# Optimization experiments

Measured on AMD Instinct MI355X. Metric: run time of the kernel, lower is better.

Reference implementation:

```python
import jax, jax.numpy as jnp
import numpy as np

INPUT_SIZE = 64
ENC_HID = 128
HIDDEN = 512
NUM_CLASSES = 8
B = 512
T = 256


def setup_inputs() -> dict:
    key = jax.random.key(0)
    ks = jax.random.split(key, 12)

    def lin(k, out_f, in_f):
        bound = 1.0 / np.sqrt(in_f)
        return jax.random.uniform(k, (out_f, in_f), jnp.float32, -bound, bound)

    def bias(k, out_f, in_f):
        bound = 1.0 / np.sqrt(in_f)
        return jax.random.uniform(k, (out_f,), jnp.float32, -bound, bound)

    return {
        "sequence": jax.random.normal(ks[0], (B, T, INPUT_SIZE), jnp.float32),
        "W1": lin(ks[1], ENC_HID, INPUT_SIZE),
        "b1": bias(ks[2], ENC_HID, INPUT_SIZE),
        "W2": lin(ks[3], HIDDEN, ENC_HID),
        "b2": bias(ks[4], HIDDEN, ENC_HID),
        "W_ih": lin(ks[5], 4 * HIDDEN, HIDDEN),
        "W_hh": lin(ks[6], 4 * HIDDEN, HIDDEN),
        "b_ih": bias(ks[7], 4 * HIDDEN, HIDDEN),
        "b_hh": bias(ks[8], 4 * HIDDEN, HIDDEN),
        "Wfc": lin(ks[9], NUM_CLASSES, HIDDEN),
        "bfc": bias(ks[10], NUM_CLASSES, HIDDEN),
    }


def reference(sequence, W1, b1, W2, b2, W_ih, W_hh, b_ih, b_hh, Wfc, bfc):
    # Encoder applied to every timestep (same math as per-step in the torch loop)
    x = jnp.einsum('bti,hi->bth', sequence, W1) + b1          # [B,T,128]
    x = jnp.where(x > 0, x, 0.01 * x)                         # LeakyReLU(0.01)
    x = jnp.einsum('bth,dh->btd', x, W2) + b2                 # [B,T,H]

    Bsz = sequence.shape[0]
    H = W_hh.shape[1]

    def step(carry, xt):
        h, c = carry
        gates = xt @ W_ih.T + b_ih + h @ W_hh.T + b_hh        # [B,4H]
        i, f, g, o = jnp.split(gates, 4, axis=-1)
        i = jax.nn.sigmoid(i)
        f = jax.nn.sigmoid(f)
        g = jnp.tanh(g)
        o = jax.nn.sigmoid(o)
        c = f * c + i * g
        h = o * jnp.tanh(c)
        return (h, c), None

    h0 = jnp.zeros((Bsz, H), x.dtype)
    (h, _), _ = jax.lax.scan(step, (h0, h0), jnp.swapaxes(x, 0, 1))  # scan over T
    return h @ Wfc.T + bfc                                    # [B,num_classes]
```

## Files before the change

kernel.cpp:

```cpp
#include <hip/hip_runtime.h>
#include <cstdint>
#include <cstddef>

#define ZB 512
#define ZT 256
#define ZIN 64
#define ZEH 128
#define ZH 512
#define ZG 2048
#define ZNC 8
#define NBLK 256

typedef __attribute__((ext_vector_type(8))) short s8v;
typedef __attribute__((ext_vector_type(4))) float f4v;
typedef unsigned short u16;
typedef unsigned int u32;
typedef unsigned long long u64;

__device__ __forceinline__ u16 f2bf(float f){
  u32 u = __builtin_bit_cast(u32, f);
  u += 0x7FFFu + ((u >> 16) & 1u);
  return (u16)(u >> 16);
}
__device__ __forceinline__ s8v pair2v(u64 a, u64 b){
  union { u64 q[2]; s8v v; } u; u.q[0] = a; u.q[1] = b; return u.v;
}
__device__ __forceinline__ size_t qoff2(int buf, int bg, int hf, int hg){
  return ((((size_t)buf * 8 + bg) * 2 + hf) * 32 + hg) * 512;
}
__device__ __forceinline__ u64 aload(const u64* p){
  return __hip_atomic_load(p, __ATOMIC_RELAXED, __HIP_MEMORY_SCOPE_AGENT);
}

__global__ __launch_bounds__(128)
void k_fold(const float* __restrict__ W_ih, const float* __restrict__ W2,
            const float* __restrict__ b2, const float* __restrict__ b_ih,
            const float* __restrict__ b_hh, u16* __restrict__ Wc,
            float* __restrict__ bc)
{
  const int r = blockIdx.x, c = threadIdx.x;
  const float* wr = W_ih + (size_t)r * ZH;
  float acc = 0.f;
  for (int k = 0; k < ZH; ++k) acc += wr[k] * W2[(size_t)k * ZEH + c];
  Wc[(size_t)r * ZEH + c] = f2bf(acc);
  __shared__ float red[128];
  float p = 0.f;
  for (int k = c; k < ZH; k += 128) p += wr[k] * b2[k];
  red[c] = p; __syncthreads();
  for (int s = 64; s > 0; s >>= 1){ if (c < s) red[c] += red[c + s]; __syncthreads(); }
  if (c == 0) bc[r] = red[0] + b_ih[r] + b_hh[r];
}

__global__ __launch_bounds__(256)
void k_cvt(const float* __restrict__ src, u16* __restrict__ dst, int n)
{
  int i = blockIdx.x * 256 + threadIdx.x;
  if (i < n) dst[i] = f2bf(src[i]);
}

__global__ __launch_bounds__(256)
void k_enc(const float* __restrict__ seq, const float* __restrict__ W1,
           const float* __restrict__ b1, u16* __restrict__ X1)
{
  __shared__ float w1s[ZEH * 65];
  __shared__ float sqs[64 * 65];
  const int tid = threadIdx.x;
  const size_t rb = (size_t)blockIdx.x * 64;
  for (int i = tid; i < ZEH * ZIN; i += 256){ int r = i >> 6, c = i & 63; w1s[r * 65 + c] = W1[i]; }
  for (int i = tid; i < 64 * ZIN; i += 256){ int r = i >> 6, c = i & 63; sqs[r * 65 + c] = seq[(rb + r) * ZIN + c]; }
  __syncthreads();
  const int cg = tid & 31, rg = tid >> 5;
  float acc[8][4];
  #pragma unroll
  for (int i = 0; i < 8; ++i){
    #pragma unroll
    for (int j = 0; j < 4; ++j) acc[i][j] = 0.f;
  }
  for (int k = 0; k < ZIN; ++k){
    float wv[4], sv[8];
    #pragma unroll
    for (int j = 0; j < 4; ++j) wv[j] = w1s[(cg * 4 + j) * 65 + k];
    #pragma unroll
    for (int i = 0; i < 8; ++i) sv[i] = sqs[(rg * 8 + i) * 65 + k];
    #pragma unroll
    for (int i = 0; i < 8; ++i){
      #pragma unroll
      for (int j = 0; j < 4; ++j) acc[i][j] += sv[i] * wv[j];
    }
  }
  #pragma unroll
  for (int i = 0; i < 8; ++i){
    ushort4 pk;
    float v0 = acc[i][0] + b1[cg * 4 + 0]; v0 = v0 > 0.f ? v0 : 0.01f * v0;
    float v1 = acc[i][1] + b1[cg * 4 + 1]; v1 = v1 > 0.f ? v1 : 0.01f * v1;
    float v2 = acc[i][2] + b1[cg * 4 + 2]; v2 = v2 > 0.f ? v2 : 0.01f * v2;
    float v3 = acc[i][3] + b1[cg * 4 + 3]; v3 = v3 > 0.f ? v3 : 0.01f * v3;
    pk.x = f2bf(v0); pk.y = f2bf(v1); pk.z = f2bf(v2); pk.w = f2bf(v3);
    int rf = (int)rb + rg * 8 + i;
    int b = rf >> 8, tt = rf & 255;
    *(ushort4*)(X1 + ((size_t)tt * ZB + b) * ZEH + cg * 4) = pk;
  }
}

__device__ __forceinline__ void qwait(const u32* flags, int gidx, u32 target)
{
  const int l = threadIdx.x & 63;
  const u32* fp = flags + ((size_t)(gidx * 32 + (l & 31))) * 16;
  long long guard = 0;
  for (;;){
    u32 v = __hip_atomic_load(fp, __ATOMIC_RELAXED, __HIP_MEMORY_SCOPE_AGENT);
    if (__ballot(v >= target) == ~0ull) break;
    __builtin_amdgcn_s_sleep(1);
    if (++guard > (1LL << 20)) break;
  }
}

__global__ __launch_bounds__(512, 1)
void k_lstm(const u16* __restrict__ X1, const u16* __restrict__ Whh,
            const u16* __restrict__ Wcf, const float* __restrict__ bc,
            const u16* __restrict__ Wfcb, const float* __restrict__ bfc,
            u16* __restrict__ hbuf, float* __restrict__ out,
            u32* __restrict__ flags)
{
  __shared__ u16 hs2[2][32 * ZH];
  const int tid = threadIdx.x;
  const int bg = (int)blockIdx.x >> 5, hg = (int)blockIdx.x & 31;
  const bool isC = (tid < 256);
  const int w = (tid >> 6) & 3, l = tid & 63;
  const int lr = l & 15, lg = l >> 4;
  const int st = tid & 255;
  const int gt = lr >> 2;

  s8v bwh[16], bwx[4];
  f4v biasv = {0.f, 0.f, 0.f, 0.f};
  float c_reg[2][2][4];
  if (isC){
    const int grow = gt * ZH + hg * 16 + w * 4 + (lr & 3);
    const u16* p = Whh + (size_t)grow * ZH + lg * 8;
    #pragma unroll
    for (int kt = 0; kt < 16; ++kt) bwh[kt] = *(const s8v*)(p + kt * 32);
    const u16* q = Wcf + (size_t)grow * ZEH + lg * 8;
    #pragma unroll
    for (int kt = 0; kt < 4; ++kt) bwx[kt] = *(const s8v*)(q + kt * 32);
    float b = bc[grow];
    biasv[0] = b; biasv[1] = b; biasv[2] = b; biasv[3] = b;
    #pragma unroll
    for (int a = 0; a < 2; ++a){
      #pragma unroll
      for (int m = 0; m < 2; ++m){
        #pragma unroll
        for (int r = 0; r < 4; ++r) c_reg[a][m][r] = 0.f;
      }
    }
  }

  if (!isC){
    const u64* src = (const u64*)(hbuf + qoff2(0, bg, 0, 0));
    u64 va[8], vb[8];
    #pragma unroll
    for (int i = 0; i < 8; ++i){
      int cc = st + i * 256;
      va[i] = aload(src + (size_t)cc * 2);
      vb[i] = aload(src + (size_t)cc * 2 + 1);
    }
    #pragma unroll
    for (int i = 0; i < 8; ++i){
      int byte = (st + i * 256) * 16;
      int swz = byte ^ (((byte >> 5) & 3) << 4);
      *(s8v*)((char*)hs2[0] + swz) = pair2v(va[i], vb[i]);
    }
  }
  __syncthreads();

  u32* flbase = flags + ((size_t)(bg * 64 + hg)) * 16;

  for (int t = 0; t < ZT; ++t){
    #pragma unroll
    for (int hf = 0; hf < 2; ++hf){
      if (isC){
        s8v ax[2][4];
        #pragma unroll
        for (int m = 0; m < 2; ++m){
          const u16* xp = X1 + ((size_t)t * ZB + (bg * 64 + hf * 32 + m * 16 + lr)) * ZEH + lg * 8;
          #pragma unroll
          for (int kt = 0; kt < 4; ++kt) ax[m][kt] = *(const s8v*)(xp + kt * 32);
        }

        const char* hb = (const char*)hs2[hf];
        f4v accm[2];
        #pragma unroll
        for (int m = 0; m < 2; ++m){
          f4v a0 = biasv;
          f4v a1 = {0.f, 0.f, 0.f, 0.f};
          #pragma unroll
          for (int kt = 0; kt < 8; ++kt){
            int byte = (2 * kt + (lg >> 1)) * 1024 + (m * 16 + lr) * 32 + (lg & 1) * 16;
            byte ^= (((byte >> 5) & 3) << 4);
            s8v av = *(const s8v*)(hb + byte);
            a0 = __builtin_amdgcn_mfma_f32_16x16x32_bf16(av, bwh[kt], a0, 0, 0, 0);
          }
          #pragma unroll
          for (int kt = 8; kt < 16; ++kt){
            int byte = (2 * kt + (lg >> 1)) * 1024 + (m * 16 + lr) * 32 + (lg & 1) * 16;
            byte ^= (((byte >> 5) & 3) << 4);
            s8v av = *(const s8v*)(hb + byte);
            a1 = __builtin_amdgcn_mfma_f32_16x16x32_bf16(av, bwh[kt], a1, 0, 0, 0);
          }
          a0 = __builtin_amdgcn_mfma_f32_16x16x32_bf16(ax[m][0], bwx[0], a0, 0, 0, 0);
          a1 = __builtin_amdgcn_mfma_f32_16x16x32_bf16(ax[m][1], bwx[1], a1, 0, 0, 0);
          a0 = __builtin_amdgcn_mfma_f32_16x16x32_bf16(ax[m][2], bwx[2], a0, 0, 0, 0);
          a1 = __builtin_amdgcn_mfma_f32_16x16x32_bf16(ax[m][3], bwx[3], a1, 0, 0, 0);
          accm[m] = a0 + a1;
        }

        u16* hdst = hbuf + qoff2((t + 1) & 1, bg, hf, hg);
        #pragma unroll
        for (int m = 0; m < 2; ++m){
          #pragma unroll
          for (int r = 0; r < 4; ++r){
            float v = accm[m][r];
            float s = (gt == 2) ? 2.f : -1.f;
            float e = __expf(v * s);
            float rc = 1.f / (1.f + e);
            float a = (gt == 2) ? (1.f - 2.f * rc) : rc;
            float f_ = __shfl_xor(a, 4);
            float g_ = __shfl_xor(a, 8);
            float o_ = __shfl_xor(a, 12);
            float cv = f_ * c_reg[hf][m][r] + a * g_;
            c_reg[hf][m][r] = cv;
            float e2 = __expf(2.f * cv);
            float hv = o_ * (1.f - 2.f / (1.f + e2));
            u32 bits = f2bf(hv);
            u32 lo = bits | (((u32)__shfl_xor((int)bits, 1)) << 16);
            u32 hi = (u32)__shfl_xor((int)lo, 2);
            if (lr == 0){
              u64 pk = (u64)lo | ((u64)hi << 32);
              __hip_atomic_store((u64*)(hdst + (size_t)(m * 16 + lg * 4 + r) * 16 + w * 4), pk,
                                 __ATOMIC_RELAXED, __HIP_MEMORY_SCOPE_AGENT);
            }
          }
        }
      } else {
        const int hfT = hf ^ 1;
        const int tf  = t + hf;
        if (tf < ZT || hf == 0){
          if (!(t == 0 && hf == 0))
            qwait(flags, bg * 2 + hfT, (u32)tf);
          const u64* src = (const u64*)(hbuf + qoff2(tf & 1, bg, hfT, 0));
          u64 va[8], vb[8];
          #pragma unroll
          for (int i = 0; i < 8; ++i){
            int cc = st + i * 256;
            va[i] = aload(src + (size_t)cc * 2);
            vb[i] = aload(src + (size_t)cc * 2 + 1);
          }
          char* dst = (char*)hs2[hf ^ 1];
          #pragma unroll
          for (int i = 0; i < 8; ++i){
            int byte = (st + i * 256) * 16;
            int swz = byte ^ (((byte >> 5) & 3) << 4);
            *(s8v*)(dst + swz) = pair2v(va[i], vb[i]);
          }
        }
      }
      __syncthreads();
      if (tid == 0)
        __hip_atomic_store(flbase + (size_t)hf * 512, (u32)(t + 1),
                           __ATOMIC_RELAXED, __HIP_MEMORY_SCOPE_AGENT);
    }
  }

  if (hg == 0){
    if (tid < 64){
      qwait(flags, bg * 2 + 0, (u32)ZT);
      qwait(flags, bg * 2 + 1, (u32)ZT);
    }
    __syncthreads();
    if (isC){
      float ob = (lr < ZNC) ? bfc[lr] : 0.f;
      f4v acc = {ob, ob, ob, ob};
      const u16* wp = Wfcb + (size_t)lr * ZH + lg * 8;
      const int hfE = w >> 1;
      const int ric = (w & 1) * 16 + lr;
      #pragma unroll
      for (int kt = 0; kt < 16; ++kt){
        int hgp = 2 * kt + (lg >> 1);
        const u64* hp = (const u64*)(hbuf + qoff2(0, bg, hfE, hgp) + (size_t)ric * 16 + (lg & 1) * 8);
        u64 a0 = aload(hp);
        u64 a1 = aload(hp + 1);
        s8v av = pair2v(a0, a1);
        s8v bv = *(const s8v*)(wp + kt * 32);
        acc = __builtin_amdgcn_mfma_f32_16x16x32_bf16(av, bv, acc, 0, 0, 0);
      }
      if (lr < ZNC){
        #pragma unroll
        for (int r = 0; r < 4; ++r)
          out[(size_t)(bg * 64 + w * 16 + lg * 4 + r) * ZNC + lr] = acc[r];
      }
    }
  }
}

extern "C" void kernel_launch(void* const* d_in, const int* in_sizes, int n_in,
                              void* d_out, int out_size, void* d_ws, size_t ws_size,
                              hipStream_t stream)
{
  const float* seq  = (const float*)d_in[0];
  const float* W1   = (const float*)d_in[1];
  const float* b1   = (const float*)d_in[2];
  const float* W2   = (const float*)d_in[3];
  const float* b2   = (const float*)d_in[4];
  const float* W_ih = (const float*)d_in[5];
  const float* W_hh = (const float*)d_in[6];
  const float* b_ih = (const float*)d_in[7];
  const float* b_hh = (const float*)d_in[8];
  const float* Wfc  = (const float*)d_in[9];
  const float* bfc  = (const float*)d_in[10];
  float* out = (float*)d_out;

  char* ws = (char*)d_ws;
  size_t off = 0;
  auto alloc = [&](size_t bytes){ void* p = ws + off; off += (bytes + 255) & ~(size_t)255; return p; };
  u16*   Wc    = (u16*)  alloc((size_t)ZG * ZEH * 2);
  float* bc    = (float*)alloc((size_t)ZG * 4);
  u16*   Whh   = (u16*)  alloc((size_t)ZG * ZH * 2);
  u16*   Wfcb  = (u16*)  alloc((size_t)16 * ZH * 2);
  u16*   X1    = (u16*)  alloc((size_t)ZB * ZT * ZEH * 2);
  u16*   hbuf  = (u16*)  alloc((size_t)2 * ZB * ZH * 2);
  u32*   flags = (u32*)  alloc((size_t)8 * 2 * 32 * 16 * 4);

  hipMemsetAsync(flags, 0, (size_t)8 * 2 * 32 * 16 * 4, stream);
  hipMemsetAsync(hbuf, 0, (size_t)ZB * ZH * 2, stream);
  hipMemsetAsync(Wfcb, 0, (size_t)16 * ZH * 2, stream);

  hipLaunchKernelGGL(k_fold, dim3(ZG), dim3(128), 0, stream, W_ih, W2, b2, b_ih, b_hh, Wc, bc);
  hipLaunchKernelGGL(k_cvt, dim3((ZG * ZH + 255) / 256), dim3(256), 0, stream, W_hh, Whh, ZG * ZH);
  hipLaunchKernelGGL(k_cvt, dim3((ZNC * ZH + 255) / 256), dim3(256), 0, stream, Wfc, Wfcb, ZNC * ZH);
  hipLaunchKernelGGL(k_enc, dim3(ZB * ZT / 64), dim3(256), 0, stream, seq, W1, b1, X1);
  hipLaunchKernelGGL(k_lstm, dim3(NBLK), dim3(512), 0, stream,
                     X1, Whh, Wc, bc, Wfcb, bfc, hbuf, out, flags);
}
```

Measured before the change: 1.756 ms.

## Publish per-wave readiness flags and prefetch flag state before barrier

```diff
diff --git a/kernel.cpp b/kernel.cpp
--- a/kernel.cpp
+++ b/kernel.cpp
@@ -29,6 +29,9 @@
   return ((((size_t)buf * 8 + bg) * 2 + hf) * 32 + hg) * 512;
 }
 __device__ __forceinline__ u64 aload(const u64* p){
+  return __hip_atomic_load(p, __ATOMIC_RELAXED, __HIP_MEMORY_SCOPE_AGENT);
+}
+__device__ __forceinline__ u32 fload(const u32* p){
   return __hip_atomic_load(p, __ATOMIC_RELAXED, __HIP_MEMORY_SCOPE_AGENT);
 }
 
@@ -102,14 +105,16 @@
   }
 }
 
-__device__ __forceinline__ void qwait(const u32* flags, int gidx, u32 target)
+__device__ __forceinline__ void qwait2(const u32* flags, int gidx, u32 target)
 {
   const int l = threadIdx.x & 63;
-  const u32* fp = flags + ((size_t)(gidx * 32 + (l & 31))) * 16;
+  const u32* f0 = flags + ((size_t)(gidx * 128 + l)) * 16;
+  const u32* f1 = f0 + 64 * 16;
   long long guard = 0;
   for (;;){
-    u32 v = __hip_atomic_load(fp, __ATOMIC_RELAXED, __HIP_MEMORY_SCOPE_AGENT);
-    if (__ballot(v >= target) == ~0ull) break;
+    u32 a = fload(f0);
+    u32 b = fload(f1);
+    if ((__ballot(a >= target) & __ballot(b >= target)) == ~0ull) break;
     __builtin_amdgcn_s_sleep(1);
     if (++guard > (1LL << 20)) break;
   }
@@ -154,6 +159,7 @@
     }
   }
 
+  u32 fp0 = 0, fp1 = 0;
   if (!isC){
     const u64* src = (const u64*)(hbuf + qoff2(0, bg, 0, 0));
     u64 va[8], vb[8];
@@ -171,8 +177,6 @@
     }
   }
   __syncthreads();
-
-  u32* flbase = flags + ((size_t)(bg * 64 + hg)) * 16;
 
   for (int t = 0; t < ZT; ++t){
     #pragma unroll
@@ -240,12 +244,19 @@
             }
           }
         }
+        asm volatile("s_waitcnt vmcnt(0)" ::: "memory");
+        __builtin_amdgcn_sched_barrier(0);
+        if (l == 0)
+          __hip_atomic_store(flags + ((size_t)((bg * 2 + hf) * 128 + hg * 4 + w)) * 16,
+                             (u32)(t + 1), __ATOMIC_RELAXED, __HIP_MEMORY_SCOPE_AGENT);
       } else {
         const int hfT = hf ^ 1;
         const int tf  = t + hf;
         if (tf < ZT || hf == 0){
-          if (!(t == 0 && hf == 0))
-            qwait(flags, bg * 2 + hfT, (u32)tf);
+          if (!(t == 0 && hf == 0)){
+            bool hit = ((__ballot(fp0 >= (u32)tf) & __ballot(fp1 >= (u32)tf)) == ~0ull);
+            if (!hit) qwait2(flags, bg * 2 + hfT, (u32)tf);
+          }
           const u64* src = (const u64*)(hbuf + qoff2(tf & 1, bg, hfT, 0));
           u64 va[8], vb[8];
           #pragma unroll
@@ -262,18 +273,20 @@
             *(s8v*)(dst + swz) = pair2v(va[i], vb[i]);
           }
         }
+        {
+          const u32* f0 = flags + ((size_t)((bg * 2 + hf) * 128 + l)) * 16;
+          fp0 = fload(f0);
+          fp1 = fload(f0 + 64 * 16);
+        }
       }
       __syncthreads();
-      if (tid == 0)
-        __hip_atomic_store(flbase + (size_t)hf * 512, (u32)(t + 1),
-                           __ATOMIC_RELAXED, __HIP_MEMORY_SCOPE_AGENT);
     }
   }
 
   if (hg == 0){
     if (tid < 64){
-      qwait(flags, bg * 2 + 0, (u32)ZT);
-      qwait(flags, bg * 2 + 1, (u32)ZT);
+      qwait2(flags, bg * 2 + 0, (u32)ZT);
+      qwait2(flags, bg * 2 + 1, (u32)ZT);
     }
     __syncthreads();
     if (isC){
@@ -327,9 +340,9 @@
   u16*   Wfcb  = (u16*)  alloc((size_t)16 * ZH * 2);
   u16*   X1    = (u16*)  alloc((size_t)ZB * ZT * ZEH * 2);
   u16*   hbuf  = (u16*)  alloc((size_t)2 * ZB * ZH * 2);
-  u32*   flags = (u32*)  alloc((size_t)8 * 2 * 32 * 16 * 4);
-
-  hipMemsetAsync(flags, 0, (size_t)8 * 2 * 32 * 16 * 4, stream);
+  u32*   flags = (u32*)  alloc((size_t)8 * 2 * 128 * 64);
+
+  hipMemsetAsync(flags, 0, (size_t)8 * 2 * 128 * 64, stream);
   hipMemsetAsync(hbuf, 0, (size_t)ZB * ZH * 2, stream);
   hipMemsetAsync(Wfcb, 0, (size_t)16 * ZH * 2, stream);
 
```

New measurement: 2.468 ms. 40.6% more time.

## Per-wave atomic flag increments and split LDS staging to shorten the LSTM step sync

Applied to the files above, without the earlier changes.

```diff
diff --git a/kernel.cpp b/kernel.cpp
--- a/kernel.cpp
+++ b/kernel.cpp
@@ -30,6 +30,9 @@
 }
 __device__ __forceinline__ u64 aload(const u64* p){
   return __hip_atomic_load(p, __ATOMIC_RELAXED, __HIP_MEMORY_SCOPE_AGENT);
+}
+__device__ __forceinline__ float rcpf(float x){
+  return __builtin_amdgcn_rcpf(x);
 }
 
 __global__ __launch_bounds__(128)
@@ -115,6 +118,10 @@
   }
 }
 
+#define RAWBAR() do{ asm volatile("s_waitcnt lgkmcnt(0)" ::: "memory"); \
+                     __builtin_amdgcn_s_barrier();                      \
+                     __builtin_amdgcn_sched_barrier(0); }while(0)
+
 __global__ __launch_bounds__(512, 1)
 void k_lstm(const u16* __restrict__ X1, const u16* __restrict__ Whh,
             const u16* __restrict__ Wcf, const float* __restrict__ bc,
@@ -154,38 +161,34 @@
     }
   }
 
-  if (!isC){
-    const u64* src = (const u64*)(hbuf + qoff2(0, bg, 0, 0));
-    u64 va[8], vb[8];
-    #pragma unroll
-    for (int i = 0; i < 8; ++i){
-      int cc = st + i * 256;
-      va[i] = aload(src + (size_t)cc * 2);
-      vb[i] = aload(src + (size_t)cc * 2 + 1);
-    }
-    #pragma unroll
-    for (int i = 0; i < 8; ++i){
-      int byte = (st + i * 256) * 16;
-      int swz = byte ^ (((byte >> 5) & 3) << 4);
-      *(s8v*)((char*)hs2[0] + swz) = pair2v(va[i], vb[i]);
-    }
-  }
+  u64 va[8], vb[8];
+  #pragma unroll
+  for (int i = 0; i < 8; ++i){ va[i] = 0; vb[i] = 0; }
   __syncthreads();
 
-  u32* flbase = flags + ((size_t)(bg * 64 + hg)) * 16;
-
   for (int t = 0; t < ZT; ++t){
     #pragma unroll
     for (int hf = 0; hf < 2; ++hf){
+      s8v ax[2][4];
       if (isC){
-        s8v ax[2][4];
         #pragma unroll
         for (int m = 0; m < 2; ++m){
           const u16* xp = X1 + ((size_t)t * ZB + (bg * 64 + hf * 32 + m * 16 + lr)) * ZEH + lg * 8;
           #pragma unroll
           for (int kt = 0; kt < 4; ++kt) ax[m][kt] = *(const s8v*)(xp + kt * 32);
         }
-
+      } else {
+        char* dst = (char*)hs2[hf];
+        #pragma unroll
+        for (int i = 0; i < 8; ++i){
+          int byte = (st + i * 256) * 16;
+          int swz = byte ^ (((byte >> 5) & 3) << 4);
+          *(s8v*)(dst + swz) = pair2v(va[i], vb[i]);
+        }
+      }
+      RAWBAR();
+
+      if (isC){
         const char* hb = (const char*)hs2[hf];
         f4v accm[2];
         #pragma unroll
@@ -221,7 +224,7 @@
             float v = accm[m][r];
             float s = (gt == 2) ? 2.f : -1.f;
             float e = __expf(v * s);
-            float rc = 1.f / (1.f + e);
+            float rc = rcpf(1.f + e);
             float a = (gt == 2) ? (1.f - 2.f * rc) : rc;
             float f_ = __shfl_xor(a, 4);
             float g_ = __shfl_xor(a, 8);
@@ -229,7 +232,7 @@
             float cv = f_ * c_reg[hf][m][r] + a * g_;
             c_reg[hf][m][r] = cv;
             float e2 = __expf(2.f * cv);
-            float hv = o_ * (1.f - 2.f / (1.f + e2));
+            float hv = o_ * (1.f - 2.f * rcpf(1.f + e2));
             u32 bits = f2bf(hv);
             u32 lo = bits | (((u32)__shfl_xor((int)bits, 1)) << 16);
             u32 hi = (u32)__shfl_xor((int)lo, 2);
@@ -240,40 +243,33 @@
             }
           }
         }
+        asm volatile("s_waitcnt vmcnt(0)" ::: "memory");
+        __builtin_amdgcn_sched_barrier(0);
+        if (l == 0)
+          __hip_atomic_fetch_add(flags + ((size_t)((bg * 2 + hf) * 32 + hg)) * 16,
+                                 1u, __ATOMIC_RELAXED, __HIP_MEMORY_SCOPE_AGENT);
       } else {
-        const int hfT = hf ^ 1;
-        const int tf  = t + hf;
-        if (tf < ZT || hf == 0){
-          if (!(t == 0 && hf == 0))
-            qwait(flags, bg * 2 + hfT, (u32)tf);
-          const u64* src = (const u64*)(hbuf + qoff2(tf & 1, bg, hfT, 0));
-          u64 va[8], vb[8];
+        const int hfN = hf ^ 1;
+        const int tfN = t + hf;
+        if (!(t == ZT - 1 && hf == 1)){
+          if (tfN > 0) qwait(flags, bg * 2 + hfN, (u32)(4 * tfN));
+          const u64* src = (const u64*)(hbuf + qoff2(tfN & 1, bg, hfN, 0));
           #pragma unroll
           for (int i = 0; i < 8; ++i){
             int cc = st + i * 256;
             va[i] = aload(src + (size_t)cc * 2);
             vb[i] = aload(src + (size_t)cc * 2 + 1);
           }
-          char* dst = (char*)hs2[hf ^ 1];
-          #pragma unroll
-          for (int i = 0; i < 8; ++i){
-            int byte = (st + i * 256) * 16;
-            int swz = byte ^ (((byte >> 5) & 3) << 4);
-            *(s8v*)(dst + swz) = pair2v(va[i], vb[i]);
-          }
-        }
-      }
-      __syncthreads();
-      if (tid == 0)
-        __hip_atomic_store(flbase + (size_t)hf * 512, (u32)(t + 1),
-                           __ATOMIC_RELAXED, __HIP_MEMORY_SCOPE_AGENT);
+        }
+      }
+      RAWBAR();
     }
   }
 
   if (hg == 0){
     if (tid < 64){
-      qwait(flags, bg * 2 + 0, (u32)ZT);
-      qwait(flags, bg * 2 + 1, (u32)ZT);
+      qwait(flags, bg * 2 + 0, (u32)(4 * ZT));
+      qwait(flags, bg * 2 + 1, (u32)(4 * ZT));
     }
     __syncthreads();
     if (isC){
```

Result: slower. 2.521 ms (+43.6%).

## Repartition LSTM across 16 batch groups with 1024-thread blocks and fast reciprocals

Applied to the files above, without the earlier changes.

```diff
diff --git a/kernel.cpp b/kernel.cpp
--- a/kernel.cpp
+++ b/kernel.cpp
@@ -25,11 +25,14 @@
 __device__ __forceinline__ s8v pair2v(u64 a, u64 b){
   union { u64 q[2]; s8v v; } u; u.q[0] = a; u.q[1] = b; return u.v;
 }
-__device__ __forceinline__ size_t qoff2(int buf, int bg, int hf, int hg){
-  return ((((size_t)buf * 8 + bg) * 2 + hf) * 32 + hg) * 512;
+__device__ __forceinline__ size_t qoff3(int buf, int bg, int hf, int ch){
+  return ((((size_t)buf * 16 + bg) * 2 + hf) * 32 + ch) * 256;
 }
 __device__ __forceinline__ u64 aload(const u64* p){
   return __hip_atomic_load(p, __ATOMIC_RELAXED, __HIP_MEMORY_SCOPE_AGENT);
+}
+__device__ __forceinline__ float rcpf(float x){
+  return __builtin_amdgcn_rcpf(x);
 }
 
 __global__ __launch_bounds__(128)
@@ -105,7 +108,7 @@
 __device__ __forceinline__ void qwait(const u32* flags, int gidx, u32 target)
 {
   const int l = threadIdx.x & 63;
-  const u32* fp = flags + ((size_t)(gidx * 32 + (l & 31))) * 16;
+  const u32* fp = flags + ((size_t)(gidx * 16 + (l & 15))) * 16;
   long long guard = 0;
   for (;;){
     u32 v = __hip_atomic_load(fp, __ATOMIC_RELAXED, __HIP_MEMORY_SCOPE_AGENT);
@@ -115,27 +118,27 @@
   }
 }
 
-__global__ __launch_bounds__(512, 1)
+__global__ __launch_bounds__(1024, 1)
 void k_lstm(const u16* __restrict__ X1, const u16* __restrict__ Whh,
             const u16* __restrict__ Wcf, const float* __restrict__ bc,
             const u16* __restrict__ Wfcb, const float* __restrict__ bfc,
             u16* __restrict__ hbuf, float* __restrict__ out,
             u32* __restrict__ flags)
 {
-  __shared__ u16 hs2[2][32 * ZH];
+  __shared__ u16 hs2[2][16 * ZH];
   const int tid = threadIdx.x;
-  const int bg = (int)blockIdx.x >> 5, hg = (int)blockIdx.x & 31;
-  const bool isC = (tid < 256);
-  const int w = (tid >> 6) & 3, l = tid & 63;
+  const int bg = (int)blockIdx.x >> 4, hg = (int)blockIdx.x & 15;
+  const bool isC = (tid < 512);
+  const int w = (tid >> 6) & 7, l = tid & 63;
   const int lr = l & 15, lg = l >> 4;
-  const int st = tid & 255;
+  const int st = tid & 511;
   const int gt = lr >> 2;
 
   s8v bwh[16], bwx[4];
   f4v biasv = {0.f, 0.f, 0.f, 0.f};
-  float c_reg[2][2][4];
+  float c_reg[2][4];
   if (isC){
-    const int grow = gt * ZH + hg * 16 + w * 4 + (lr & 3);
+    const int grow = gt * ZH + hg * 32 + w * 4 + (lr & 3);
     const u16* p = Whh + (size_t)grow * ZH + lg * 8;
     #pragma unroll
     for (int kt = 0; kt < 16; ++kt) bwh[kt] = *(const s8v*)(p + kt * 32);
@@ -147,97 +150,84 @@
     #pragma unroll
     for (int a = 0; a < 2; ++a){
       #pragma unroll
-      for (int m = 0; m < 2; ++m){
-        #pragma unroll
-        for (int r = 0; r < 4; ++r) c_reg[a][m][r] = 0.f;
-      }
+      for (int r = 0; r < 4; ++r) c_reg[a][r] = 0.f;
     }
   }
 
   if (!isC){
-    const u64* src = (const u64*)(hbuf + qoff2(0, bg, 0, 0));
-    u64 va[8], vb[8];
-    #pragma unroll
-    for (int i = 0; i < 8; ++i){
-      int cc = st + i * 256;
+    const u64* src = (const u64*)(hbuf + qoff3(0, bg, 0, 0));
+    u64 va[2], vb[2];
+    #pragma unroll
+    for (int i = 0; i < 2; ++i){
+      int cc = st + i * 512;
       va[i] = aload(src + (size_t)cc * 2);
       vb[i] = aload(src + (size_t)cc * 2 + 1);
     }
     #pragma unroll
-    for (int i = 0; i < 8; ++i){
-      int byte = (st + i * 256) * 16;
+    for (int i = 0; i < 2; ++i){
+      int byte = (st + i * 512) * 16;
       int swz = byte ^ (((byte >> 5) & 3) << 4);
       *(s8v*)((char*)hs2[0] + swz) = pair2v(va[i], vb[i]);
     }
   }
   __syncthreads();
 
-  u32* flbase = flags + ((size_t)(bg * 64 + hg)) * 16;
-
   for (int t = 0; t < ZT; ++t){
     #pragma unroll
     for (int hf = 0; hf < 2; ++hf){
       if (isC){
-        s8v ax[2][4];
+        s8v ax[4];
+        {
+          const u16* xp = X1 + ((size_t)t * ZB + (bg * 32 + hf * 16 + lr)) * ZEH + lg * 8;
+          #pragma unroll
+          for (int kt = 0; kt < 4; ++kt) ax[kt] = *(const s8v*)(xp + kt * 32);
+        }
+
+        const char* hb = (const char*)hs2[hf];
+        f4v a0 = biasv;
+        f4v a1 = {0.f, 0.f, 0.f, 0.f};
         #pragma unroll
-        for (int m = 0; m < 2; ++m){
-          const u16* xp = X1 + ((size_t)t * ZB + (bg * 64 + hf * 32 + m * 16 + lr)) * ZEH + lg * 8;
-          #pragma unroll
-          for (int kt = 0; kt < 4; ++kt) ax[m][kt] = *(const s8v*)(xp + kt * 32);
-        }
-
-        const char* hb = (const char*)hs2[hf];
-        f4v accm[2];
+        for (int kt = 0; kt < 8; ++kt){
+          int byte = (2 * kt + (lg >> 1)) * 512 + lr * 32 + (lg & 1) * 16;
+          byte ^= ((lr & 3) << 4);
+          s8v av = *(const s8v*)(hb + byte);
+          a0 = __builtin_amdgcn_mfma_f32_16x16x32_bf16(av, bwh[kt], a0, 0, 0, 0);
+        }
         #pragma unroll
-        for (int m = 0; m < 2; ++m){
-          f4v a0 = biasv;
-          f4v a1 = {0.f, 0.f, 0.f, 0.f};
-          #pragma unroll
-          for (int kt = 0; kt < 8; ++kt){
-            int byte = (2 * kt + (lg >> 1)) * 1024 + (m * 16 + lr) * 32 + (lg & 1) * 16;
-            byte ^= (((byte >> 5) & 3) << 4);
-            s8v av = *(const s8v*)(hb + byte);
-            a0 = __builtin_amdgcn_mfma_f32_16x16x32_bf16(av, bwh[kt], a0, 0, 0, 0);
-          }
-          #pragma unroll
-          for (int kt = 8; kt < 16; ++kt){
-            int byte = (2 * kt + (lg >> 1)) * 1024 + (m * 16 + lr) * 32 + (lg & 1) * 16;
-            byte ^= (((byte >> 5) & 3) << 4);
-            s8v av = *(const s8v*)(hb + byte);
-            a1 = __builtin_amdgcn_mfma_f32_16x16x32_bf16(av, bwh[kt], a1, 0, 0, 0);
-          }
-          a0 = __builtin_amdgcn_mfma_f32_16x16x32_bf16(ax[m][0], bwx[0], a0, 0, 0, 0);
-          a1 = __builtin_amdgcn_mfma_f32_16x16x32_bf16(ax[m][1], bwx[1], a1, 0, 0, 0);
-          a0 = __builtin_amdgcn_mfma_f32_16x16x32_bf16(ax[m][2], bwx[2], a0, 0, 0, 0);
-          a1 = __builtin_amdgcn_mfma_f32_16x16x32_bf16(ax[m][3], bwx[3], a1, 0, 0, 0);
-          accm[m] = a0 + a1;
-        }
-
-        u16* hdst = hbuf + qoff2((t + 1) & 1, bg, hf, hg);
+        for (int kt = 8; kt < 16; ++kt){
+          int byte = (2 * kt + (lg >> 1)) * 512 + lr * 32 + (lg & 1) * 16;
+          byte ^= ((lr & 3) << 4);
+          s8v av = *(const s8v*)(hb + byte);
+          a1 = __builtin_amdgcn_mfma_f32_16x16x32_bf16(av, bwh[kt], a1, 0, 0, 0);
+        }
+        a0 = __builtin_amdgcn_mfma_f32_16x16x32_bf16(ax[0], bwx[0], a0, 0, 0, 0);
+        a1 = __builtin_amdgcn_mfma_f32_16x16x32_bf16(ax[1], bwx[1], a1, 0, 0, 0);
+        a0 = __builtin_amdgcn_mfma_f32_16x16x32_bf16(ax[2], bwx[2], a0, 0, 0, 0);
+        a1 = __builtin_amdgcn_mfma_f32_16x16x32_bf16(ax[3], bwx[3], a1, 0, 0, 0);
+        f4v acc = a0 + a1;
+
+        u16* hdst = hbuf + qoff3((t + 1) & 1, bg, hf, hg * 2 + (w >> 2));
         #pragma unroll
-        for (int m = 0; m < 2; ++m){
-          #pragma unroll
-          for (int r = 0; r < 4; ++r){
-            float v = accm[m][r];
-            float s = (gt == 2) ? 2.f : -1.f;
-            float e = __expf(v * s);
-            float rc = 1.f / (1.f + e);
-            float a = (gt == 2) ? (1.f - 2.f * rc) : rc;
-            float f_ = __shfl_xor(a, 4);
-            float g_ = __shfl_xor(a, 8);
-            float o_ = __shfl_xor(a, 12);
-            float cv = f_ * c_reg[hf][m][r] + a * g_;
-            c_reg[hf][m][r] = cv;
-            float e2 = __expf(2.f * cv);
-            float hv = o_ * (1.f - 2.f / (1.f + e2));
-            u32 bits = f2bf(hv);
-            u32 lo = bits | (((u32)__shfl_xor((int)bits, 1)) << 16);
-            u32 hi = (u32)__shfl_xor((int)lo, 2);
-            if (lr == 0){
-              u64 pk = (u64)lo | ((u64)hi << 32);
-              __hip_atomic_store((u64*)(hdst + (size_t)(m * 16 + lg * 4 + r) * 16 + w * 4), pk,
-                                 __ATOMIC_RELAXED, __HIP_MEMORY_SCOPE_AGENT);
-            }
+        for (int r = 0; r < 4; ++r){
+          float v = acc[r];
+          float s = (gt == 2) ? 2.f : -1.f;
+          float e = __expf(v * s);
+          float rc = rcpf(1.f + e);
+          float a = (gt == 2) ? (1.f - 2.f * rc) : rc;
+          float f_ = __shfl_xor(a, 4);
+          float g_ = __shfl_xor(a, 8);
+          float o_ = __shfl_xor(a, 12);
+          float cv = f_ * c_reg[hf][r] + a * g_;
+          c_reg[hf][r] = cv;
+          float e2 = __expf(2.f * cv);
+          float hv = o_ * (1.f - 2.f * rcpf(1.f + e2));
+          u32 bits = f2bf(hv);
+          u32 lo = bits | (((u32)__shfl_xor((int)bits, 1)) << 16);
+          u32 hi = (u32)__shfl_xor((int)lo, 2);
+          if (lr == 0){
+            u64 pk = (u64)lo | ((u64)hi << 32);
+            __hip_atomic_store((u64*)(hdst + (size_t)(lg * 4 + r) * 16 + (w & 3) * 4), pk,
+                               __ATOMIC_RELAXED, __HIP_MEMORY_SCOPE_AGENT);
           }
         }
       } else {
@@ -246,18 +236,18 @@
         if (tf < ZT || hf == 0){
           if (!(t == 0 && hf == 0))
             qwait(flags, bg * 2 + hfT, (u32)tf);
-          const u64* src = (const u64*)(hbuf + qoff2(tf & 1, bg, hfT, 0));
-          u64 va[8], vb[8];
+          const u64* src = (const u64*)(hbuf + qoff3(tf & 1, bg, hfT, 0));
+          u64 va[2], vb[2];
           #pragma unroll
-          for (int i = 0; i < 8; ++i){
-            int cc = st + i * 256;
+          for (int i = 0; i < 2; ++i){
+            int cc = st + i * 512;
             va[i] = aload(src + (size_t)cc * 2);
             vb[i] = aload(src + (size_t)cc * 2 + 1);
           }
           char* dst = (char*)hs2[hf ^ 1];
           #pragma unroll
-          for (int i = 0; i < 8; ++i){
-            int byte = (st + i * 256) * 16;
+          for (int i = 0; i < 2; ++i){
+            int byte = (st + i * 512) * 16;
             int swz = byte ^ (((byte >> 5) & 3) << 4);
             *(s8v*)(dst + swz) = pair2v(va[i], vb[i]);
           }
@@ -265,8 +255,8 @@
       }
       __syncthreads();
       if (tid == 0)
-        __hip_atomic_store(flbase + (size_t)hf * 512, (u32)(t + 1),
-                           __ATOMIC_RELAXED, __HIP_MEMORY_SCOPE_AGENT);
+        __hip_atomic_store(flags + ((size_t)((bg * 2 + hf) * 16 + hg)) * 16,
+                           (u32)(t + 1), __ATOMIC_RELAXED, __HIP_MEMORY_SCOPE_AGENT);
     }
   }
 
@@ -276,16 +266,14 @@
       qwait(flags, bg * 2 + 1, (u32)ZT);
     }
     __syncthreads();
-    if (isC){
+    if (isC && w < 2){
       float ob = (lr < ZNC) ? bfc[lr] : 0.f;
       f4v acc = {ob, ob, ob, ob};
       const u16* wp = Wfcb + (size_t)lr * ZH + lg * 8;
-      const int hfE = w >> 1;
-      const int ric = (w & 1) * 16 + lr;
       #pragma unroll
       for (int kt = 0; kt < 16; ++kt){
-        int hgp = 2 * kt + (lg >> 1);
-        const u64* hp = (const u64*)(hbuf + qoff2(0, bg, hfE, hgp) + (size_t)ric * 16 + (lg & 1) * 8);
+        int ch = 2 * kt + (lg >> 1);
+        const u64* hp = (const u64*)(hbuf + qoff3(0, bg, w, ch)) + lr * 4 + (lg & 1) * 2;
         u64 a0 = aload(hp);
         u64 a1 = aload(hp + 1);
         s8v av = pair2v(a0, a1);
@@ -295,7 +283,7 @@
       if (lr < ZNC){
         #pragma unroll
         for (int r = 0; r < 4; ++r)
-          out[(size_t)(bg * 64 + w * 16 + lg * 4 + r) * ZNC + lr] = acc[r];
+          out[(size_t)(bg * 32 + w * 16 + lg * 4 + r) * ZNC + lr] = acc[r];
       }
     }
   }
@@ -327,9 +315,9 @@
   u16*   Wfcb  = (u16*)  alloc((size_t)16 * ZH * 2);
   u16*   X1    = (u16*)  alloc((size_t)ZB * ZT * ZEH * 2);
   u16*   hbuf  = (u16*)  alloc((size_t)2 * ZB * ZH * 2);
-  u32*   flags = (u32*)  alloc((size_t)8 * 2 * 32 * 16 * 4);
-
-  hipMemsetAsync(flags, 0, (size_t)8 * 2 * 32 * 16 * 4, stream);
+  u32*   flags = (u32*)  alloc((size_t)16 * 2 * 16 * 64);
+
+  hipMemsetAsync(flags, 0, (size_t)16 * 2 * 16 * 64, stream);
   hipMemsetAsync(hbuf, 0, (size_t)ZB * ZH * 2, stream);
   hipMemsetAsync(Wfcb, 0, (size_t)16 * ZH * 2, stream);
 
@@ -337,6 +325,6 @@
   hipLaunchKernelGGL(k_cvt, dim3((ZG * ZH + 255) / 256), dim3(256), 0, stream, W_hh, Whh, ZG * ZH);
   hipLaunchKernelGGL(k_cvt, dim3((ZNC * ZH + 255) / 256), dim3(256), 0, stream, Wfc, Wfcb, ZNC * ZH);
   hipLaunchKernelGGL(k_enc, dim3(ZB * ZT / 64), dim3(256), 0, stream, seq, W1, b1, X1);
-  hipLaunchKernelGGL(k_lstm, dim3(NBLK), dim3(512), 0, stream,
+  hipLaunchKernelGGL(k_lstm, dim3(NBLK), dim3(1024), 0, stream,
                      X1, Whh, Wc, bc, Wfcb, bfc, hbuf, out, flags);
 }
```

Result: slower. 2.231 ms (+27.1%).
